# Optimization experiments

Measured on AMD Instinct MI355X. Metric: run time of the kernel, lower is better.

The kernel has to match this reference:

```python
import jax, jax.numpy as jnp
import numpy as np
from jax import lax

B, D, N = 16, 128, 8192   # batch, channels (dim), sequence length
KS = 5                    # causal conv kernel size
W = 128                   # local attention window size (N % W == 0 -> autopad no-op)
EPS = 1e-5


def setup_inputs() -> dict:
    key = jax.random.key(0)
    ks = jax.random.split(key, 10)
    s = 0.05
    return {
        "x":   jax.random.normal(ks[0], (B, D, N), jnp.float32),
        "q_w": jax.random.normal(ks[1], (D, D, KS), jnp.float32) * s,
        "q_b": jnp.zeros((D,), jnp.float32),
        "k_w": jax.random.normal(ks[2], (D, D, KS), jnp.float32) * s,
        "k_b": jnp.zeros((D,), jnp.float32),
        "v_w": jax.random.normal(ks[3], (D, D, KS), jnp.float32) * s,
        "v_b": jnp.zeros((D,), jnp.float32),
        "o_w": jax.random.normal(ks[4], (D, D, 1), jnp.float32) * s,
        "o_b": jnp.zeros((D,), jnp.float32),
        "gamma": jnp.ones((D,), jnp.float32),
        "beta":  jnp.zeros((D,), jnp.float32),
    }


def causal_conv1d(x, w, b):
    # x: (B, C, N), w: (O, I, K)  -- left-pad by K-1 for causality
    k = w.shape[-1]
    y = lax.conv_general_dilated(x, w, (1,), [(k - 1, 0)],
                                 dimension_numbers=('NCH', 'OIH', 'NCH'))
    return y + b[None, :, None]


def apply_rotary(q, k):
    # Sinusoidal rotary embeddings (local-attention lib applies these when dim is passed).
    n, d = q.shape[-2], q.shape[-1]
    inv_freq = 1.0 / (10000.0 ** (jnp.arange(0, d, 2, dtype=jnp.float32) / d))
    t = jnp.arange(n, dtype=jnp.float32)
    freqs = t[:, None] * inv_freq[None, :]           # (n, d/2)
    freqs = jnp.concatenate([freqs, freqs], axis=-1)  # (n, d)
    cos, sin = jnp.cos(freqs), jnp.sin(freqs)

    def rot_half(x):
        x1, x2 = jnp.split(x, 2, axis=-1)
        return jnp.concatenate([-x2, x1], axis=-1)

    return q * cos + rot_half(q) * sin, k * cos + rot_half(k) * sin


def local_causal_attention(q, k, v, w):
    # q,k,v: (B, N, D); windowed causal attention, look_backward=1, look_forward=0
    b, n, d = q.shape
    nw = n // w
    q, k = apply_rotary(q, k)
    scale = d ** -0.5
    bq = q.reshape(b, nw, w, d) * scale
    bk = k.reshape(b, nw, w, d)
    bv = v.reshape(b, nw, w, d)

    # look_around: each window attends to [previous window, current window]
    def with_prev(t):  # (b, nw, w, d) -> (b, nw, 2w, d)
        prev = jnp.pad(t, ((0, 0), (1, 0), (0, 0), (0, 0)))[:, :-1]
        return jnp.concatenate([prev, t], axis=2)

    kk = with_prev(bk)
    vv = with_prev(bv)

    # bucketed positions; pad positions marked -1 (masked out)
    t = jnp.arange(n, dtype=jnp.int32).reshape(nw, w)
    t_prev = jnp.pad(t, ((1, 0), (0, 0)), constant_values=-1)[:-1]
    bt = jnp.concatenate([t_prev, t], axis=1)          # (nw, 2w)
    mask = (t[:, :, None] >= bt[:, None, :]) & (bt[:, None, :] >= 0)  # (nw, w, 2w)

    sim = jnp.einsum('bnid,bnjd->bnij', bq, kk)        # (b, nw, w, 2w)
    neg = jnp.finfo(sim.dtype).min
    sim = jnp.where(mask[None], sim, neg)
    attn = jax.nn.softmax(sim, axis=-1)
    out = jnp.einsum('bnij,bnjd->bnid', attn, vv)
    return out.reshape(b, n, d)


def reference(x, q_w, q_b, k_w, k_b, v_w, v_b, o_w, o_b, gamma, beta):
    q = causal_conv1d(x, q_w, q_b)   # (B, D, N)
    k = causal_conv1d(x, k_w, k_b)
    v = causal_conv1d(x, v_w, v_b)
    a = local_causal_attention(q.transpose(0, 2, 1),
                               k.transpose(0, 2, 1),
                               v.transpose(0, 2, 1), W)
    y = a.transpose(0, 2, 1)          # (B, D, N)
    # 1x1 conv
    y = jnp.einsum('oi,bin->bon', o_w[:, :, 0], y) + o_b[None, :, None]
    # BatchNorm1d, training-mode (batch statistics, biased variance)
    mean = jnp.mean(y, axis=(0, 2), keepdims=True)
    var = jnp.var(y, axis=(0, 2), keepdims=True)
    y = (y - mean) * lax.rsqrt(var + EPS)
    return y * gamma[None, :, None] + beta[None, :, None]
```

## Files before the change

### kernel.cpp

```cpp
#include <hip/hip_runtime.h>
#include <math.h>

#define B_   16
#define D_   128
#define N_   8192
#define EPS_ 1e-5f
#define SCALE_ 0.08838834764831845f
#define NEG_ -3.4028235e38f

typedef _Float16 half8 __attribute__((ext_vector_type(8)));
typedef float f32x16 __attribute__((ext_vector_type(16)));
#define MFMA32(a,b,c) __builtin_amdgcn_mfma_f32_32x32x16_f16(a,b,c,0,0,0)

#define OFF_QA    0UL
#define OFF_K     8388608UL
#define OFF_VT    16777216UL
#define OFF_AT    25165824UL
#define OFF_ROPE  33554432UL
#define OFF_WB    34603008UL
#define OFF_INVF  34725888UL
#define OFF_W2H   34725952UL
#define OFF_B2    34734144UL
#define OFF_MEANP 34734272UL
#define OFF_SP    34767040UL
#define OFF_MEAN  38961344UL
#define OFF_S     38961472UL

__device__ __forceinline__ int swz(int row, int col) {
  return row * 128 + ((((col >> 3) ^ (row & 7))) << 3) + (col & 7);
}

__global__ __launch_bounds__(64) void invf_kernel(float* __restrict__ invf) {
  int j = threadIdx.x;
  invf[j] = (float)pow(10000.0, -(double)j / 64.0);
}

__global__ __launch_bounds__(256) void rope2_kernel(const float* __restrict__ invf,
                                                    float* __restrict__ rope2) {
  int idx = blockIdx.x * 256 + threadIdx.x;
  int n = idx >> 6, j = idx & 63;
  float ph = (float)n * invf[j];
  rope2[(size_t)n * 128 + 2 * j]     = cosf(ph);
  rope2[(size_t)n * 128 + 2 * j + 1] = sinf(ph);
}

__global__ __launch_bounds__(128) void prepack_kernel(
    const float* __restrict__ qw, const float* __restrict__ kw,
    const float* __restrict__ vw, _Float16* __restrict__ WB) {
  int o = blockIdx.x, t = blockIdx.y, c = blockIdx.z, i = threadIdx.x;
  const float* w = (c == 0) ? qw : (c == 1) ? kw : vw;
  float v = w[(o * 128 + i) * 5 + t] * (c == 0 ? SCALE_ : 1.f);
  WB[(((size_t)(c * 5 + t) * 128 + o) * 128) + i] = (_Float16)v;
}

__global__ __launch_bounds__(256, 2) void conv_kernel(
    const float* __restrict__ x, const _Float16* __restrict__ WB,
    const float* __restrict__ qb, const float* __restrict__ kb_,
    const float* __restrict__ vb,
    _Float16* __restrict__ qo, _Float16* __restrict__ ko,
    _Float16* __restrict__ vT)
{
  __shared__ _Float16 xs[132 * 128];
  __shared__ _Float16 wb[128 * 128];
  const int b = blockIdx.y, n0 = blockIdx.x * 128;
  const int tid = threadIdx.x;
  const int lane = tid & 63, wq = tid >> 6;
  const int l31 = lane & 31, h = lane >> 5;

  {
    int i = tid >> 1, g = tid & 1;
    const float* xrow = x + ((size_t)b * 128 + i) * (size_t)N_;
    int j0 = g * 66;
    for (int m = 0; m < 66; ++m) {
      int j = j0 + m, n = n0 - 4 + j;
      float v = (n >= 0) ? xrow[n] : 0.f;
      xs[swz(j, i)] = (_Float16)v;
    }
  }

  for (int c = 0; c < 3; ++c) {
    f32x16 acc[4];
    #pragma unroll
    for (int nt = 0; nt < 4; ++nt)
      #pragma unroll
      for (int u = 0; u < 16; ++u) acc[nt][u] = 0.f;

    for (int t = 0; t < 5; ++t) {
      __syncthreads();
      {
        const _Float16* src = WB + ((size_t)(c * 5 + t) << 14);
        #pragma unroll
        for (int m = 0; m < 8; ++m) {
          int idx = m * 256 + tid;
          int o = idx >> 4, ip = idx & 15;
          half8 v = *(const half8*)(src + o * 128 + ip * 8);
          *(half8*)(wb + o * 128 + ((ip ^ (o & 7)) << 3)) = v;
        }
      }
      __syncthreads();
      const int arow = wq * 32 + l31 + t;
      const int r7a = arow & 7;
      #pragma unroll
      for (int kb2 = 0; kb2 < 8; ++kb2) {
        half8 av = *(const half8*)(xs + arow * 128 + ((((kb2 * 2 + h) ^ r7a)) << 3));
        #pragma unroll
        for (int nt = 0; nt < 4; ++nt) {
          int o = nt * 32 + l31;
          half8 bv = *(const half8*)(wb + o * 128 + ((((kb2 * 2 + h) ^ (o & 7))) << 3));
          acc[nt] = MFMA32(av, bv, acc[nt]);
        }
      }
    }

    if (c < 2) {
      const float* bias = (c == 0) ? qb : kb_;
      float bsc = (c == 0) ? SCALE_ : 1.f;
      _Float16* outp = (c == 0) ? qo : ko;
      #pragma unroll
      for (int nt = 0; nt < 4; ++nt) {
        int o = nt * 32 + l31;
        float bv = bias[o] * bsc;
        #pragma unroll
        for (int reg = 0; reg < 16; ++reg) {
          int pos = wq * 32 + (reg & 3) + 8 * (reg >> 2) + 4 * h;
          outp[((size_t)b * N_ + n0 + pos) * 128 + o] = (_Float16)(acc[nt][reg] + bv);
        }
      }
    } else {
      __syncthreads();
      #pragma unroll
      for (int nt = 0; nt < 4; ++nt) {
        int o = nt * 32 + l31;
        float bv = vb[o];
        #pragma unroll
        for (int reg = 0; reg < 16; ++reg) {
          int pos = wq * 32 + (reg & 3) + 8 * (reg >> 2) + 4 * h;
          xs[swz(o, pos)] = (_Float16)(acc[nt][reg] + bv);
        }
      }
      __syncthreads();
      int o2 = tid >> 1, g2 = tid & 1;
      _Float16* dst = vT + ((size_t)b * 128 + o2) * (size_t)N_ + n0 + g2 * 64;
      #pragma unroll
      for (int m = 0; m < 8; ++m) {
        int pos = g2 * 64 + m * 8;
        half8 v = *(const half8*)(xs + o2 * 128 + ((((pos >> 3) ^ (o2 & 7))) << 3));
        *(half8*)(dst + m * 8) = v;
      }
    }
  }
}

__device__ __forceinline__ void stage_rot(const _Float16* __restrict__ src_base,
                                          _Float16* __restrict__ dst,
                                          const float* __restrict__ rope2,
                                          int nbase, int tid)
{
  int row = tid >> 2, p = tid & 3;
  const _Float16* src = src_base + (size_t)row * 128;
  const float* rp = rope2 + ((size_t)(nbase + row)) * 128 + p * 32;
  half8 lo0 = *(const half8*)(src + p * 16);
  half8 lo1 = *(const half8*)(src + p * 16 + 8);
  half8 hi0 = *(const half8*)(src + 64 + p * 16);
  half8 hi1 = *(const half8*)(src + 64 + p * 16 + 8);
  half8 olo0, olo1, ohi0, ohi1;
  #pragma unroll
  for (int u = 0; u < 8; ++u) {
    float c0 = rp[2 * u], s0 = rp[2 * u + 1];
    float c1 = rp[16 + 2 * u], s1 = rp[16 + 2 * u + 1];
    float xl0 = (float)lo0[u], xh0 = (float)hi0[u];
    float xl1 = (float)lo1[u], xh1 = (float)hi1[u];
    olo0[u] = (_Float16)(xl0 * c0 - xh0 * s0);
    ohi0[u] = (_Float16)(xh0 * c0 + xl0 * s0);
    olo1[u] = (_Float16)(xl1 * c1 - xh1 * s1);
    ohi1[u] = (_Float16)(xh1 * c1 + xl1 * s1);
  }
  int r7 = row & 7;
  *(half8*)(dst + row * 128 + (((p * 2)     ^ r7) << 3)) = olo0;
  *(half8*)(dst + row * 128 + (((p * 2 + 1) ^ r7) << 3)) = olo1;
  *(half8*)(dst + row * 128 + (((8 + p * 2) ^ r7) << 3)) = ohi0;
  *(half8*)(dst + row * 128 + (((9 + p * 2) ^ r7) << 3)) = ohi1;
}

__device__ __forceinline__ void stage_vT(const _Float16* __restrict__ vsrc,
                                         _Float16* __restrict__ dst, int tid)
{
  int d = tid >> 2, p = tid & 3;
  const _Float16* src = vsrc + (size_t)d * (size_t)N_;
  int r7 = d & 7;
  #pragma unroll
  for (int m = 0; m < 4; ++m) {
    int kp = m * 32 + p * 8;
    half8 v = *(const half8*)(src + kp);
    *(half8*)(dst + d * 128 + ((((kp >> 3) ^ r7)) << 3)) = v;
  }
}

__global__ __launch_bounds__(512, 2) void attn_kernel(
    const _Float16* __restrict__ q, const _Float16* __restrict__ k,
    const _Float16* __restrict__ vT, const float* __restrict__ rope2,
    _Float16* __restrict__ aout, _Float16* __restrict__ aTout)
{
  __shared__ _Float16 q_s[128 * 128];
  __shared__ _Float16 k_s[128 * 128];
  __shared__ _Float16 vT_s[128 * 128];
  __shared__ _Float16 P_s[128 * 128];
  __shared__ float red_m[2][128];
  __shared__ float red_s[2][128];

  const int b = blockIdx.y, w = blockIdx.x;
  const int tid = threadIdx.x, lane = tid & 63, wid = tid >> 6;
  const int wr = wid >> 1, wc = wid & 1;
  const int l31 = lane & 31, h = lane >> 5;

  stage_rot(q + ((size_t)b * N_ + w * 128) * 128, q_s, rope2, w * 128, tid);

  float mrun[16], lrun[16];
  f32x16 O[2];
  #pragma unroll
  for (int r = 0; r < 16; ++r) { mrun[r] = NEG_; lrun[r] = 0.f; O[0][r] = 0.f; O[1][r] = 0.f; }

  const int qrow = wr * 32 + l31;
  const int r7q = qrow & 7;
  int rowof[16];
  #pragma unroll
  for (int r = 0; r < 16; ++r) rowof[r] = wr * 32 + (r & 3) + 8 * (r >> 2) + 4 * h;

  for (int ch = (w == 0 ? 1 : 0); ch < 2; ++ch) {
    int kv0 = w * 128 - 128 + ch * 128;
    __syncthreads();
    stage_rot(k + ((size_t)b * N_ + kv0) * 128, k_s, rope2, kv0, tid);
    stage_vT(vT + (size_t)b * 128 * (size_t)N_ + kv0, vT_s, tid);
    __syncthreads();

    f32x16 sim[2];
    #pragma unroll
    for (int r = 0; r < 16; ++r) { sim[0][r] = 0.f; sim[1][r] = 0.f; }
    #pragma unroll
    for (int kb2 = 0; kb2 < 8; ++kb2) {
      half8 av = *(const half8*)(q_s + qrow * 128 + ((((kb2 * 2 + h) ^ r7q)) << 3));
      #pragma unroll
      for (int nt = 0; nt < 2; ++nt) {
        int krow = wc * 64 + nt * 32 + l31;
        half8 bv = *(const half8*)(k_s + krow * 128 + ((((kb2 * 2 + h) ^ (krow & 7))) << 3));
        sim[nt] = MFMA32(av, bv, sim[nt]);
      }
    }
    if (ch == 1) {
      #pragma unroll
      for (int nt = 0; nt < 2; ++nt) {
        int col = wc * 64 + nt * 32 + l31;
        #pragma unroll
        for (int r = 0; r < 16; ++r)
          if (col > rowof[r]) sim[nt][r] = NEG_;
      }
    }

    float pm[16];
    #pragma unroll
    for (int r = 0; r < 16; ++r) pm[r] = fmaxf(sim[0][r], sim[1][r]);
    #pragma unroll
    for (int m = 1; m <= 16; m <<= 1)
      #pragma unroll
      for (int r = 0; r < 16; ++r) pm[r] = fmaxf(pm[r], __shfl_xor(pm[r], m));
    if (l31 == 0) {
      #pragma unroll
      for (int r = 0; r < 16; ++r) red_m[wc][rowof[r]] = pm[r];
    }
    __syncthreads();

    float scale[16], ps[16];
    #pragma unroll
    for (int r = 0; r < 16; ++r) {
      float mc = fmaxf(red_m[0][rowof[r]], red_m[1][rowof[r]]);
      float mn = fmaxf(mrun[r], mc);
      scale[r] = __expf(mrun[r] - mn);
      mrun[r] = mn;
      ps[r] = 0.f;
    }
    #pragma unroll
    for (int nt = 0; nt < 2; ++nt) {
      int col = wc * 64 + nt * 32 + l31;
      #pragma unroll
      for (int r = 0; r < 16; ++r) {
        float p = __expf(sim[nt][r] - mrun[r]);
        ps[r] += p;
        P_s[swz(rowof[r], col)] = (_Float16)p;
      }
    }
    #pragma unroll
    for (int m = 1; m <= 16; m <<= 1)
      #pragma unroll
      for (int r = 0; r < 16; ++r) ps[r] += __shfl_xor(ps[r], m);
    if (l31 == 0) {
      #pragma unroll
      for (int r = 0; r < 16; ++r) red_s[wc][rowof[r]] = ps[r];
    }
    __syncthreads();

    #pragma unroll
    for (int r = 0; r < 16; ++r) {
      float ss = red_s[0][rowof[r]] + red_s[1][rowof[r]];
      lrun[r] = lrun[r] * scale[r] + ss;
      O[0][r] *= scale[r];
      O[1][r] *= scale[r];
    }

    #pragma unroll
    for (int kb2 = 0; kb2 < 8; ++kb2) {
      half8 pa = *(const half8*)(P_s + qrow * 128 + ((((kb2 * 2 + h) ^ r7q)) << 3));
      #pragma unroll
      for (int nt = 0; nt < 2; ++nt) {
        int drow = wc * 64 + nt * 32 + l31;
        half8 bv = *(const half8*)(vT_s + drow * 128 + ((((kb2 * 2 + h) ^ (drow & 7))) << 3));
        O[nt] = MFMA32(pa, bv, O[nt]);
      }
    }
  }

  #pragma unroll
  for (int nt = 0; nt < 2; ++nt) {
    int col = wc * 64 + nt * 32 + l31;
    #pragma unroll
    for (int r = 0; r < 16; ++r) {
      float inv = 1.f / lrun[r];
      _Float16 val = (_Float16)(O[nt][r] * inv);
      aout[((size_t)b * N_ + w * 128 + rowof[r]) * 128 + col] = val;
      q_s[swz(col, rowof[r])] = val;
    }
  }
  __syncthreads();
  {
    int d = tid >> 2, part = tid & 3;
    _Float16* dst = aTout + ((size_t)b * 128 + d) * (size_t)N_ + w * 128 + part * 32;
    #pragma unroll
    for (int mm = 0; mm < 4; ++mm) {
      int mb = part * 4 + mm;
      *(half8*)(dst + mm * 8) = *(const half8*)(q_s + d * 128 + ((mb ^ (d & 7)) << 3));
    }
  }
}

__global__ __launch_bounds__(256, 2) void stats_kernel(
    const _Float16* __restrict__ aT, float* __restrict__ Sp, float* __restrict__ meanp)
{
  __shared__ _Float16 ts[128 * 64];
  const int bk = blockIdx.x;
  const int b = bk >> 4;
  const int nbase = (bk & 15) * 512;
  const int tid = threadIdx.x, lane = tid & 63, wv = tid >> 6;
  const int l31 = lane & 31, h = lane >> 5;

  f32x16 acc[4];
  #pragma unroll
  for (int jt = 0; jt < 4; ++jt)
    #pragma unroll
    for (int u = 0; u < 16; ++u) acc[jt][u] = 0.f;
  float csum = 0.f;

  const int i2 = tid >> 1, part = tid & 1;
  const int ia = wv * 32 + l31;
  for (int sc = 0; sc < 8; ++sc) {
    __syncthreads();
    {
      const _Float16* src = aT + ((size_t)b * 128 + i2) * (size_t)N_ + nbase + sc * 64 + part * 32;
      #pragma unroll
      for (int mm = 0; mm < 4; ++mm) {
        half8 v = *(const half8*)(src + mm * 8);
        int mb = part * 4 + mm;
        *(half8*)(ts + i2 * 64 + (((mb ^ (i2 & 7))) << 3)) = v;
      }
    }
    __syncthreads();
    if (tid < 128) {
      #pragma unroll
      for (int mb = 0; mb < 8; ++mb) {
        half8 v = *(const half8*)(ts + tid * 64 + (((mb ^ (tid & 7))) << 3));
        #pragma unroll
        for (int u = 0; u < 8; ++u) csum += (float)v[u];
      }
    }
    #pragma unroll
    for (int kk = 0; kk < 4; ++kk) {
      int mb = kk * 2 + h;
      half8 av = *(const half8*)(ts + ia * 64 + (((mb ^ (ia & 7))) << 3));
      #pragma unroll
      for (int jt = 0; jt < 4; ++jt) {
        int jb = jt * 32 + l31;
        half8 bvv = *(const half8*)(ts + jb * 64 + (((mb ^ (jb & 7))) << 3));
        acc[jt] = MFMA32(av, bvv, acc[jt]);
      }
    }
  }
  float* dst = Sp + (size_t)bk * 16384;
  #pragma unroll
  for (int jt = 0; jt < 4; ++jt)
    #pragma unroll
    for (int r = 0; r < 16; ++r) {
      int i = wv * 32 + (r & 3) + 8 * (r >> 2) + 4 * h;
      dst[i * 128 + jt * 32 + l31] = acc[jt][r];
    }
  if (tid < 128) meanp[bk * 128 + tid] = csum;
}

__global__ __launch_bounds__(256) void reduce_kernel(
    const float* __restrict__ Sp, const float* __restrict__ meanp,
    float* __restrict__ S, float* __restrict__ mean)
{
  const int e = blockIdx.x * 256 + threadIdx.x;
  float s = 0.f;
  for (int bk = 0; bk < 256; ++bk) s += Sp[(size_t)bk * 16384 + e];
  S[e] = s;
  if (blockIdx.x == 0 && threadIdx.x < 128) {
    float ms = 0.f;
    for (int bk = 0; bk < 256; ++bk) ms += meanp[bk * 128 + threadIdx.x];
    mean[threadIdx.x] = ms * (1.f / (float)(B_ * N_));
  }
}

__global__ __launch_bounds__(128) void fold_kernel(
    const float* __restrict__ S, const float* __restrict__ mean,
    const float* __restrict__ ow, const float* __restrict__ gamma,
    const float* __restrict__ beta,
    _Float16* __restrict__ w2h, float* __restrict__ b2)
{
  __shared__ float wo_s[128];
  __shared__ float qred[2], dred[2];
  const int o = blockIdx.x, i = threadIdx.x;
  const int lane = i & 63, wv = i >> 6;
  float wi = ow[o * 128 + i];
  wo_s[i] = wi;
  __syncthreads();
  const float* Srow = S + i * 128;
  float t = 0.f;
  #pragma unroll 8
  for (int j = 0; j < 128; ++j) t = fmaf(Srow[j], wo_s[j], t);
  float quad = wi * t;
  float dm = wi * mean[i];
  #pragma unroll
  for (int m = 1; m <= 32; m <<= 1) {
    quad += __shfl_xor(quad, m);
    dm   += __shfl_xor(dm, m);
  }
  if (lane == 0) { qred[wv] = quad; dred[wv] = dm; }
  __syncthreads();
  float quadT = qred[0] + qred[1];
  float dmT   = dred[0] + dred[1];
  float var = quadT * (1.f / (float)(B_ * N_)) - dmT * dmT;
  var = fmaxf(var, 0.f);
  float sc = gamma[o] * rsqrtf(var + EPS_);
  if (i == 0) b2[o] = beta[o] - sc * dmT;
  w2h[o * 128 + i] = (_Float16)(sc * wi);
}

__global__ __launch_bounds__(256, 2) void out_kernel(
    const _Float16* __restrict__ a, const _Float16* __restrict__ w2h,
    const float* __restrict__ b2, float* __restrict__ out)
{
  __shared__ _Float16 a_s[128 * 128];
  __shared__ _Float16 w_s[128 * 128];
  const int b = blockIdx.y, n0 = blockIdx.x * 128;
  const int tid = threadIdx.x, lane = tid & 63, wv = tid >> 6;
  const int l31 = lane & 31, h = lane >> 5;
  {
    int row = tid >> 1, part = tid & 1;
    const _Float16* asrc = a + ((size_t)b * N_ + n0 + row) * 128 + part * 64;
    const _Float16* wsrc = w2h + row * 128 + part * 64;
    #pragma unroll
    for (int mm = 0; mm < 8; ++mm) {
      int mb = part * 8 + mm;
      int off = row * 128 + ((mb ^ (row & 7)) << 3);
      *(half8*)(a_s + off) = *(const half8*)(asrc + mm * 8);
      *(half8*)(w_s + off) = *(const half8*)(wsrc + mm * 8);
    }
  }
  __syncthreads();
  f32x16 acc[4];
  #pragma unroll
  for (int pt = 0; pt < 4; ++pt)
    #pragma unroll
    for (int u = 0; u < 16; ++u) acc[pt][u] = 0.f;
  const int orow = wv * 32 + l31;
  #pragma unroll
  for (int kk = 0; kk < 8; ++kk) {
    int mb = kk * 2 + h;
    half8 av = *(const half8*)(w_s + orow * 128 + ((mb ^ (orow & 7)) << 3));
    #pragma unroll
    for (int pt = 0; pt < 4; ++pt) {
      int prow = pt * 32 + l31;
      half8 bvv = *(const half8*)(a_s + prow * 128 + ((mb ^ (prow & 7)) << 3));
      acc[pt] = MFMA32(av, bvv, acc[pt]);
    }
  }
  float bias[16];
  int orows[16];
  #pragma unroll
  for (int r = 0; r < 16; ++r) {
    orows[r] = wv * 32 + (r & 3) + 8 * (r >> 2) + 4 * h;
    bias[r] = b2[orows[r]];
  }
  #pragma unroll
  for (int pt = 0; pt < 4; ++pt)
    #pragma unroll
    for (int r = 0; r < 16; ++r)
      out[((size_t)b * 128 + orows[r]) * N_ + n0 + pt * 32 + l31] = acc[pt][r] + bias[r];
}

extern "C" void kernel_launch(void* const* d_in, const int* in_sizes, int n_in,
                              void* d_out, int out_size, void* d_ws, size_t ws_size,
                              hipStream_t stream)
{
  const float* x     = (const float*)d_in[0];
  const float* qw    = (const float*)d_in[1];
  const float* qb    = (const float*)d_in[2];
  const float* kw    = (const float*)d_in[3];
  const float* kb    = (const float*)d_in[4];
  const float* vw    = (const float*)d_in[5];
  const float* vb    = (const float*)d_in[6];
  const float* ow    = (const float*)d_in[7];
  const float* ob    = (const float*)d_in[8];  (void)ob;
  const float* gamma = (const float*)d_in[9];
  const float* beta  = (const float*)d_in[10];
  float* out = (float*)d_out;
  float* ws  = (float*)d_ws;

  _Float16* q    = (_Float16*)(ws + OFF_QA);
  _Float16* k    = (_Float16*)(ws + OFF_K);
  _Float16* vT   = (_Float16*)(ws + OFF_VT);
  _Float16* aT   = (_Float16*)(ws + OFF_AT);
  float* rope2   = ws + OFF_ROPE;
  _Float16* WB   = (_Float16*)(ws + OFF_WB);
  float* invf    = ws + OFF_INVF;
  _Float16* w2h  = (_Float16*)(ws + OFF_W2H);
  float* b2      = ws + OFF_B2;
  float* meanp   = ws + OFF_MEANP;
  float* Sp      = ws + OFF_SP;
  float* mean    = ws + OFF_MEAN;
  float* S       = ws + OFF_S;

  invf_kernel<<<1, 64, 0, stream>>>(invf);
  rope2_kernel<<<(N_ * 64) / 256, 256, 0, stream>>>(invf, rope2);
  prepack_kernel<<<dim3(128, 5, 3), 128, 0, stream>>>(qw, kw, vw, WB);

  conv_kernel<<<dim3(N_ / 128, B_), 256, 0, stream>>>(x, WB, qb, kb, vb, q, k, vT);

  attn_kernel<<<dim3(N_ / 128, B_), 512, 0, stream>>>(q, k, vT, rope2,
                                                      q , aT);

  stats_kernel<<<256, 256, 0, stream>>>(aT, Sp, meanp);
  reduce_kernel<<<64, 256, 0, stream>>>(Sp, meanp, S, mean);
  fold_kernel<<<128, 128, 0, stream>>>(S, mean, ow, gamma, beta, w2h, b2);

  out_kernel<<<dim3(N_ / 128, B_), 256, 0, stream>>>(q, w2h, b2, out);
}
```

Baseline: 422.2 us.

## Pre-transpose x to fp16 and double-buffer conv weights in larger tiles

Adds a separate kernel that transposes x into a position-major fp16 buffer with 132-wide padded rows. The conv kernel then fills shared memory with contiguous vector loads instead of strided per-element scalar loads. The conv kernel now handles 256 positions with 512 threads, uses padding instead of an XOR swizzle, and double-buffers the weight tiles. The next tap's weights are prefetched into registers during the MFMAs, which cuts the barriers per tap from two to one. The cost is an extra launch plus a round trip of x through global memory, and much more shared memory per block (about 136 KB), which may limit occupancy.

```diff
diff --git a/kernel.cpp b/kernel.cpp
--- a/kernel.cpp
+++ b/kernel.cpp
@@ -9,6 +9,7 @@
 #define NEG_ -3.4028235e38f
 
 typedef _Float16 half8 __attribute__((ext_vector_type(8)));
+typedef _Float16 half4 __attribute__((ext_vector_type(4)));
 typedef float f32x16 __attribute__((ext_vector_type(16)));
 #define MFMA32(a,b,c) __builtin_amdgcn_mfma_f32_32x32x16_f16(a,b,c,0,0,0)
 
@@ -16,15 +17,16 @@
 #define OFF_K     8388608UL
 #define OFF_VT    16777216UL
 #define OFF_AT    25165824UL
-#define OFF_ROPE  33554432UL
-#define OFF_WB    34603008UL
-#define OFF_INVF  34725888UL
-#define OFF_W2H   34725952UL
-#define OFF_B2    34734144UL
-#define OFF_MEANP 34734272UL
-#define OFF_SP    34767040UL
-#define OFF_MEAN  38961344UL
-#define OFF_S     38961472UL
+#define OFF_XT    33554432UL
+#define OFF_ROPE  42205184UL
+#define OFF_WB    43253760UL
+#define OFF_INVF  43380480UL
+#define OFF_W2H   43380544UL
+#define OFF_B2    43388736UL
+#define OFF_MEANP 43388864UL
+#define OFF_SP    43421632UL
+#define OFF_MEAN  47615936UL
+#define OFF_S     47616064UL
 
 __device__ __forceinline__ int swz(int row, int col) {
   return row * 128 + ((((col >> 3) ^ (row & 7))) << 3) + (col & 7);
@@ -50,104 +52,161 @@
   int o = blockIdx.x, t = blockIdx.y, c = blockIdx.z, i = threadIdx.x;
   const float* w = (c == 0) ? qw : (c == 1) ? kw : vw;
   float v = w[(o * 128 + i) * 5 + t] * (c == 0 ? SCALE_ : 1.f);
-  WB[(((size_t)(c * 5 + t) * 128 + o) * 128) + i] = (_Float16)v;
-}
-
-__global__ __launch_bounds__(256, 2) void conv_kernel(
-    const float* __restrict__ x, const _Float16* __restrict__ WB,
+  WB[((size_t)(c * 5 + t) * 128 + o) * 132 + i] = (_Float16)v;
+}
+
+__global__ __launch_bounds__(256) void xpose_kernel(
+    const float* __restrict__ x, _Float16* __restrict__ xT)
+{
+  __shared__ _Float16 ls[64 * 132];
+  const int b = blockIdx.y, n0 = blockIdx.x * 64;
+  const int tid = threadIdx.x;
+  {
+    const int q = tid & 3;
+    #pragma unroll
+    for (int pass = 0; pass < 2; ++pass) {
+      int d = (tid >> 2) + pass * 64;
+      const float* src = x + ((size_t)b * 128 + d) * (size_t)N_ + n0;
+      #pragma unroll
+      for (int m = 0; m < 4; ++m) {
+        int p = m * 16 + q * 4;
+        float4 v = *(const float4*)(src + p);
+        ls[(p + 0) * 132 + d] = (_Float16)v.x;
+        ls[(p + 1) * 132 + d] = (_Float16)v.y;
+        ls[(p + 2) * 132 + d] = (_Float16)v.z;
+        ls[(p + 3) * 132 + d] = (_Float16)v.w;
+      }
+    }
+  }
+  __syncthreads();
+  {
+    const int p = tid >> 2, c4 = tid & 3;
+    _Float16* dst = xT + ((size_t)b * N_ + n0 + p) * 132;
+    #pragma unroll
+    for (int mm = 0; mm < 8; ++mm) {
+      int cc = (c4 + mm * 4) * 4;
+      *(half4*)(dst + cc) = *(const half4*)(ls + p * 132 + cc);
+    }
+  }
+}
+
+__global__ __launch_bounds__(512, 2) void conv_kernel(
+    const _Float16* __restrict__ xT, const _Float16* __restrict__ WB,
     const float* __restrict__ qb, const float* __restrict__ kb_,
     const float* __restrict__ vb,
     _Float16* __restrict__ qo, _Float16* __restrict__ ko,
     _Float16* __restrict__ vT)
 {
-  __shared__ _Float16 xs[132 * 128];
-  __shared__ _Float16 wb[128 * 128];
-  const int b = blockIdx.y, n0 = blockIdx.x * 128;
+  __shared__ _Float16 xs[260 * 132];
+  __shared__ _Float16 wbuf[2][128 * 132];
+  const int b = blockIdx.y, n0 = blockIdx.x * 256;
   const int tid = threadIdx.x;
   const int lane = tid & 63, wq = tid >> 6;
   const int l31 = lane & 31, h = lane >> 5;
 
   {
-    int i = tid >> 1, g = tid & 1;
-    const float* xrow = x + ((size_t)b * 128 + i) * (size_t)N_;
-    int j0 = g * 66;
-    for (int m = 0; m < 66; ++m) {
-      int j = j0 + m, n = n0 - 4 + j;
-      float v = (n >= 0) ? xrow[n] : 0.f;
-      xs[swz(j, i)] = (_Float16)v;
-    }
-  }
+    const _Float16* src = xT + ((size_t)b * N_ + n0 - 4) * 132;
+    #pragma unroll
+    for (int kk = 0; kk < 9; ++kk) {
+      int u = kk * 512 + tid;
+      if (u < 4290) *(half8*)(xs + u * 8) = *(const half8*)(src + u * 8);
+    }
+    #pragma unroll
+    for (int kk = 0; kk < 5; ++kk) {
+      int u = kk * 512 + tid;
+      if (u < 2112) *(half8*)(&wbuf[0][0] + u * 8) = *(const half8*)(WB + u * 8);
+    }
+  }
+  __syncthreads();
+  if (n0 == 0) {
+    xs[tid] = (_Float16)0.f;
+    if (tid < 16) xs[512 + tid] = (_Float16)0.f;
+  }
+  __syncthreads();
+
+  int rowof[16];
+  #pragma unroll
+  for (int r = 0; r < 16; ++r) rowof[r] = (r & 3) + 8 * (r >> 2) + 4 * h;
+
+  f32x16 acc[4];
+  #pragma unroll
+  for (int nt = 0; nt < 4; ++nt)
+    #pragma unroll
+    for (int u = 0; u < 16; ++u) acc[nt][u] = 0.f;
 
   for (int c = 0; c < 3; ++c) {
-    f32x16 acc[4];
-    #pragma unroll
-    for (int nt = 0; nt < 4; ++nt)
-      #pragma unroll
-      for (int u = 0; u < 16; ++u) acc[nt][u] = 0.f;
-
     for (int t = 0; t < 5; ++t) {
-      __syncthreads();
-      {
-        const _Float16* src = WB + ((size_t)(c * 5 + t) << 14);
+      const int ct = c * 5 + t;
+      const int cur = ct & 1;
+      const bool more = ct < 14;
+      half8 wreg[5];
+      if (more) {
+        const _Float16* wsrc = WB + (size_t)(ct + 1) * 16896;
         #pragma unroll
-        for (int m = 0; m < 8; ++m) {
-          int idx = m * 256 + tid;
-          int o = idx >> 4, ip = idx & 15;
-          half8 v = *(const half8*)(src + o * 128 + ip * 8);
-          *(half8*)(wb + o * 128 + ((ip ^ (o & 7)) << 3)) = v;
+        for (int kk = 0; kk < 5; ++kk) {
+          int u = kk * 512 + tid;
+          if (u < 2112) wreg[kk] = *(const half8*)(wsrc + u * 8);
         }
       }
-      __syncthreads();
-      const int arow = wq * 32 + l31 + t;
-      const int r7a = arow & 7;
+      const int abase = (wq * 32 + l31 + t) * 132;
+      const _Float16* wb_ = &wbuf[cur][0];
       #pragma unroll
       for (int kb2 = 0; kb2 < 8; ++kb2) {
-        half8 av = *(const half8*)(xs + arow * 128 + ((((kb2 * 2 + h) ^ r7a)) << 3));
+        half8 av = *(const half8*)(xs + abase + (kb2 * 2 + h) * 8);
         #pragma unroll
         for (int nt = 0; nt < 4; ++nt) {
           int o = nt * 32 + l31;
-          half8 bv = *(const half8*)(wb + o * 128 + ((((kb2 * 2 + h) ^ (o & 7))) << 3));
+          half8 bv = *(const half8*)(wb_ + o * 132 + (kb2 * 2 + h) * 8);
           acc[nt] = MFMA32(av, bv, acc[nt]);
         }
       }
-    }
-
-    if (c < 2) {
-      const float* bias = (c == 0) ? qb : kb_;
-      float bsc = (c == 0) ? SCALE_ : 1.f;
-      _Float16* outp = (c == 0) ? qo : ko;
-      #pragma unroll
-      for (int nt = 0; nt < 4; ++nt) {
-        int o = nt * 32 + l31;
-        float bv = bias[o] * bsc;
+      if (more) {
+        _Float16* wdst = &wbuf[cur ^ 1][0];
         #pragma unroll
-        for (int reg = 0; reg < 16; ++reg) {
-          int pos = wq * 32 + (reg & 3) + 8 * (reg >> 2) + 4 * h;
-          outp[((size_t)b * N_ + n0 + pos) * 128 + o] = (_Float16)(acc[nt][reg] + bv);
+        for (int kk = 0; kk < 5; ++kk) {
+          int u = kk * 512 + tid;
+          if (u < 2112) *(half8*)(wdst + u * 8) = wreg[kk];
         }
       }
-    } else {
+      if (t == 4 && c < 2) {
+        const float* bias = (c == 0) ? qb : kb_;
+        const float bsc = (c == 0) ? SCALE_ : 1.f;
+        _Float16* outp = (c == 0) ? qo : ko;
+        #pragma unroll
+        for (int nt = 0; nt < 4; ++nt) {
+          int o = nt * 32 + l31;
+          float bv = bias[o] * bsc;
+          #pragma unroll
+          for (int r = 0; r < 16; ++r) {
+            int pos = wq * 32 + rowof[r];
+            outp[((size_t)b * N_ + n0 + pos) * 128 + o] = (_Float16)(acc[nt][r] + bv);
+          }
+          #pragma unroll
+          for (int r = 0; r < 16; ++r) acc[nt][r] = 0.f;
+        }
+      }
       __syncthreads();
-      #pragma unroll
-      for (int nt = 0; nt < 4; ++nt) {
-        int o = nt * 32 + l31;
-        float bv = vb[o];
-        #pragma unroll
-        for (int reg = 0; reg < 16; ++reg) {
-          int pos = wq * 32 + (reg & 3) + 8 * (reg >> 2) + 4 * h;
-          xs[swz(o, pos)] = (_Float16)(acc[nt][reg] + bv);
-        }
-      }
-      __syncthreads();
-      int o2 = tid >> 1, g2 = tid & 1;
-      _Float16* dst = vT + ((size_t)b * 128 + o2) * (size_t)N_ + n0 + g2 * 64;
-      #pragma unroll
-      for (int m = 0; m < 8; ++m) {
-        int pos = g2 * 64 + m * 8;
-        half8 v = *(const half8*)(xs + o2 * 128 + ((((pos >> 3) ^ (o2 & 7))) << 3));
-        *(half8*)(dst + m * 8) = v;
-      }
-    }
+    }
+  }
+
+  {
+    _Float16* vbuf = xs;
+    #pragma unroll
+    for (int nt = 0; nt < 4; ++nt) {
+      int o = nt * 32 + l31;
+      float bv = vb[o];
+      #pragma unroll
+      for (int r = 0; r < 16; ++r) {
+        int pos = wq * 32 + rowof[r];
+        vbuf[o * 260 + pos] = (_Float16)(acc[nt][r] + bv);
+      }
+    }
+    __syncthreads();
+    const int o2 = tid & 127, seg = tid >> 7;
+    _Float16* dst = vT + ((size_t)b * 128 + o2) * (size_t)N_ + n0 + seg * 64;
+    #pragma unroll
+    for (int m = 0; m < 16; ++m)
+      *(half4*)(dst + m * 4) = *(const half4*)(vbuf + o2 * 260 + seg * 64 + m * 4);
   }
 }
 
@@ -528,6 +587,7 @@
   _Float16* k    = (_Float16*)(ws + OFF_K);
   _Float16* vT   = (_Float16*)(ws + OFF_VT);
   _Float16* aT   = (_Float16*)(ws + OFF_AT);
+  _Float16* xT   = (_Float16*)(ws + OFF_XT);
   float* rope2   = ws + OFF_ROPE;
   _Float16* WB   = (_Float16*)(ws + OFF_WB);
   float* invf    = ws + OFF_INVF;
@@ -541,8 +601,9 @@
   invf_kernel<<<1, 64, 0, stream>>>(invf);
   rope2_kernel<<<(N_ * 64) / 256, 256, 0, stream>>>(invf, rope2);
   prepack_kernel<<<dim3(128, 5, 3), 128, 0, stream>>>(qw, kw, vw, WB);
-
-  conv_kernel<<<dim3(N_ / 128, B_), 256, 0, stream>>>(x, WB, qb, kb, vb, q, k, vT);
+  xpose_kernel<<<dim3(N_ / 64, B_), 256, 0, stream>>>(x, xT);
+
+  conv_kernel<<<dim3(N_ / 256, B_), 512, 0, stream>>>(xT, WB, qb, kb, vb, q, k, vT);
 
   attn_kernel<<<dim3(N_ / 128, B_), 512, 0, stream>>>(q, k, vT, rope2,
                                                       q , aT);
```

Result: slower. 568.0 us (+34.5%).
